# Optimization experiments

Hardware: AMD Instinct MI355X
Metric: run time of the kernel (lower is better)

The kernel has to match this reference:

```python
import jax, jax.numpy as jnp
import numpy as np

N_NODES = 50000


def gcn_conv(x, W, b, src, dst, n):
    """PyG-style GCNConv: symmetric-normalized aggregation over A + I.
    x: [N, Fin], W: [Fin, Fout], b: [Fout], src/dst: [E] int edge endpoints.
    """
    h = x @ W  # [N, Fout]
    # degree with self-loops: deg[i] = 1 + in-degree(i)
    deg = jnp.zeros((n,), dtype=h.dtype).at[dst].add(1.0) + 1.0
    dinv = jax.lax.rsqrt(deg)  # deg^-1/2
    norm_e = dinv[src] * dinv[dst]  # [E]
    # message passing: sum_j norm_ij * h_j  (plus self-loop term deg_i^-1 * h_i)
    agg = jnp.zeros_like(h).at[dst].add(h[src] * norm_e[:, None])
    agg = agg + h * (dinv * dinv)[:, None]
    return agg + b


def setup_inputs() -> dict:
    key = jax.random.key(0)
    ks = jax.random.split(key, 9)
    N, F_in, H, C = N_NODES, 128, 64, 4
    E = 1600000
    node_features = jax.random.normal(ks[0], (N, F_in), dtype=jnp.float32)
    edge_index = jax.random.randint(ks[1], (2, E), 0, N, dtype=jnp.int32)
    s1 = 1.0 / np.sqrt(F_in)
    s2 = 1.0 / np.sqrt(H)
    W1 = jax.random.uniform(ks[2], (F_in, H), jnp.float32, -s1, s1)
    b1 = jax.random.uniform(ks[3], (H,), jnp.float32, -s1, s1)
    W2 = jax.random.uniform(ks[4], (H, H), jnp.float32, -s2, s2)
    b2 = jax.random.uniform(ks[5], (H,), jnp.float32, -s2, s2)
    W3 = jax.random.uniform(ks[6], (H, C), jnp.float32, -s2, s2)
    b3 = jax.random.uniform(ks[7], (C,), jnp.float32, -s2, s2)
    return {"node_features": node_features, "edge_index": edge_index,
            "W1": W1, "b1": b1, "W2": W2, "b2": b2, "W3": W3, "b3": b3}


def reference(node_features, edge_index, W1, b1, W2, b2, W3, b3):
    n = node_features.shape[0]
    src, dst = edge_index[0], edge_index[1]
    out = jax.nn.relu(gcn_conv(node_features, W1, b1, src, dst, n))
    # layer2 applied 7 times with SHARED weights (faithful to the source)
    for _ in range(7):
        out = jax.nn.relu(gcn_conv(out, W2, b2, src, dst, n))
    out = gcn_conv(out, W3, b3, src, dst, n)
    return jax.nn.softmax(out, axis=0)  # softmax over the node dimension (dim=0)
```

## Files before the change

kernel.cpp:

```cpp
#include <hip/hip_runtime.h>
#include <hip/hip_fp16.h>
#include <math.h>
#include <float.h>


#define NPART 8
#define BPP   104

typedef float f4 __attribute__((ext_vector_type(4)));


__global__ __launch_bounds__(256) void k_count(const int* __restrict__ dst,
                                               unsigned* __restrict__ deg,
                                               int E, int chunk) {
    int part = blockIdx.x & (NPART - 1);
    int q = blockIdx.x >> 3;
    int lo = part * chunk, hi = lo + chunk;
    for (int e = q * 256 + threadIdx.x; e < E; e += 256 * BPP) {
        int d = dst[e];
        if (d >= lo && d < hi) atomicAdd(&deg[d], 1u);
    }
}

__global__ __launch_bounds__(256) void k_dinv(const unsigned* __restrict__ deg,
                                              float* __restrict__ dinv, int n) {
    int i = blockIdx.x * 256 + threadIdx.x;
    if (i < n) dinv[i] = rsqrtf(1.0f + (float)deg[i]);
}

__global__ __launch_bounds__(256) void k_scan1(const unsigned* __restrict__ deg,
                                               int* __restrict__ row_start,
                                               unsigned* __restrict__ bsum, int n) {
    __shared__ unsigned t[256];
    int i = blockIdx.x * 256 + threadIdx.x;
    unsigned v = (i < n) ? deg[i] : 0u;
    t[threadIdx.x] = v;
    __syncthreads();
    #pragma unroll
    for (int off = 1; off < 256; off <<= 1) {
        unsigned u = (threadIdx.x >= (unsigned)off) ? t[threadIdx.x - off] : 0u;
        __syncthreads();
        t[threadIdx.x] += u;
        __syncthreads();
    }
    if (i < n) row_start[i] = (int)(t[threadIdx.x] - v);
    if (threadIdx.x == 255) bsum[blockIdx.x] = t[255];
}

__global__ __launch_bounds__(256) void k_scan2(unsigned* __restrict__ bsum,
                                               int* __restrict__ row_start,
                                               int nb, int n) {
    __shared__ unsigned t[256];
    unsigned v = (threadIdx.x < (unsigned)nb) ? bsum[threadIdx.x] : 0u;
    t[threadIdx.x] = v;
    __syncthreads();
    #pragma unroll
    for (int off = 1; off < 256; off <<= 1) {
        unsigned u = (threadIdx.x >= (unsigned)off) ? t[threadIdx.x - off] : 0u;
        __syncthreads();
        t[threadIdx.x] += u;
        __syncthreads();
    }
    if (threadIdx.x < (unsigned)nb) bsum[threadIdx.x] = t[threadIdx.x] - v;
    if (threadIdx.x == 255) row_start[n] = (int)t[255];
}

__global__ __launch_bounds__(256) void k_scan3(int* __restrict__ row_start,
                                               const unsigned* __restrict__ bsum, int n) {
    int i = blockIdx.x * 256 + threadIdx.x;
    if (i < n) row_start[i] += (int)bsum[blockIdx.x];
}

__global__ __launch_bounds__(256) void k_fill(const int* __restrict__ src,
                                              const int* __restrict__ dst,
                                              const int* __restrict__ row_start,
                                              unsigned* __restrict__ cursor,
                                              int* __restrict__ csr_src,
                                              int E, int chunk) {
    int part = blockIdx.x & (NPART - 1);
    int q = blockIdx.x >> 3;
    int lo = part * chunk, hi = lo + chunk;
    for (int e = q * 256 + threadIdx.x; e < E; e += 256 * BPP) {
        int d = dst[e];
        if (d >= lo && d < hi) {
            int s = src[e];
            unsigned pos = atomicAdd(&cursor[d], 1u);
            csr_src[row_start[d] + (int)pos] = s;
        }
    }
}


__global__ __launch_bounds__(256) void k_gemm64_f32(const float* __restrict__ x,
                                                    const float* __restrict__ W,
                                                    const float* __restrict__ dinv,
                                                    __half* __restrict__ hs, int n) {
    __shared__ float Wl[128 * 64];
    {
        const f4* Wv = (const f4*)W;
        f4* Wlv = (f4*)Wl;
        for (int idx = threadIdx.x; idx < 128 * 16; idx += 256) Wlv[idx] = Wv[idx];
    }
    __syncthreads();
    int wave = threadIdx.x >> 6, lane = threadIdx.x & 63;
    int i0 = blockIdx.x * 16 + wave * 4;
    if (i0 >= n) return;
    if (i0 + 3 < n) {
        const f4* r0 = (const f4*)(x + (size_t)(i0 + 0) * 128);
        const f4* r1 = (const f4*)(x + (size_t)(i0 + 1) * 128);
        const f4* r2 = (const f4*)(x + (size_t)(i0 + 2) * 128);
        const f4* r3 = (const f4*)(x + (size_t)(i0 + 3) * 128);
        float a0 = 0.f, a1 = 0.f, a2 = 0.f, a3 = 0.f;
        #pragma unroll
        for (int k4 = 0; k4 < 32; ++k4) {
            f4 v0 = __builtin_nontemporal_load(&r0[k4]);
            f4 v1 = __builtin_nontemporal_load(&r1[k4]);
            f4 v2 = __builtin_nontemporal_load(&r2[k4]);
            f4 v3 = __builtin_nontemporal_load(&r3[k4]);
            float w0 = Wl[(k4 * 4 + 0) * 64 + lane];
            float w1 = Wl[(k4 * 4 + 1) * 64 + lane];
            float w2 = Wl[(k4 * 4 + 2) * 64 + lane];
            float w3 = Wl[(k4 * 4 + 3) * 64 + lane];
            a0 += v0.x * w0 + v0.y * w1 + v0.z * w2 + v0.w * w3;
            a1 += v1.x * w0 + v1.y * w1 + v1.z * w2 + v1.w * w3;
            a2 += v2.x * w0 + v2.y * w1 + v2.z * w2 + v2.w * w3;
            a3 += v3.x * w0 + v3.y * w1 + v3.z * w2 + v3.w * w3;
        }
        hs[(size_t)(i0 + 0) * 64 + lane] = __float2half(a0 * dinv[i0 + 0]);
        hs[(size_t)(i0 + 1) * 64 + lane] = __float2half(a1 * dinv[i0 + 1]);
        hs[(size_t)(i0 + 2) * 64 + lane] = __float2half(a2 * dinv[i0 + 2]);
        hs[(size_t)(i0 + 3) * 64 + lane] = __float2half(a3 * dinv[i0 + 3]);
    } else {
        for (int i = i0; i < n && i < i0 + 4; ++i) {
            const f4* r = (const f4*)(x + (size_t)i * 128);
            float acc = 0.f;
            #pragma unroll
            for (int k4 = 0; k4 < 32; ++k4) {
                f4 v = r[k4];
                acc += v.x * Wl[(k4 * 4 + 0) * 64 + lane];
                acc += v.y * Wl[(k4 * 4 + 1) * 64 + lane];
                acc += v.z * Wl[(k4 * 4 + 2) * 64 + lane];
                acc += v.w * Wl[(k4 * 4 + 3) * 64 + lane];
            }
            hs[(size_t)i * 64 + lane] = __float2half(acc * dinv[i]);
        }
    }
}


__global__ __launch_bounds__(256) void k_gemm64_f16(const __half* __restrict__ xh,
                                                    const float* __restrict__ W,
                                                    const float* __restrict__ dinv,
                                                    __half* __restrict__ hs, int n) {
    __shared__ float Wl[64 * 64];
    {
        const f4* Wv = (const f4*)W;
        f4* Wlv = (f4*)Wl;
        for (int idx = threadIdx.x; idx < 64 * 16; idx += 256) Wlv[idx] = Wv[idx];
    }
    __syncthreads();
    int wave = threadIdx.x >> 6, lane = threadIdx.x & 63;
    int i0 = blockIdx.x * 16 + wave * 4;
    if (i0 >= n) return;
    if (i0 + 3 < n) {
        const unsigned* r0 = (const unsigned*)(xh + (size_t)(i0 + 0) * 64);
        const unsigned* r1 = (const unsigned*)(xh + (size_t)(i0 + 1) * 64);
        const unsigned* r2 = (const unsigned*)(xh + (size_t)(i0 + 2) * 64);
        const unsigned* r3 = (const unsigned*)(xh + (size_t)(i0 + 3) * 64);
        float a0 = 0.f, a1 = 0.f, a2 = 0.f, a3 = 0.f;
        #pragma unroll
        for (int k2 = 0; k2 < 32; ++k2) {
            unsigned u0 = __builtin_nontemporal_load(&r0[k2]);
            unsigned u1 = __builtin_nontemporal_load(&r1[k2]);
            unsigned u2 = __builtin_nontemporal_load(&r2[k2]);
            unsigned u3 = __builtin_nontemporal_load(&r3[k2]);
            float w0 = Wl[(k2 * 2 + 0) * 64 + lane];
            float w1 = Wl[(k2 * 2 + 1) * 64 + lane];
            float2 v0 = __half22float2(*(__half2*)&u0);
            float2 v1 = __half22float2(*(__half2*)&u1);
            float2 v2 = __half22float2(*(__half2*)&u2);
            float2 v3 = __half22float2(*(__half2*)&u3);
            a0 += v0.x * w0 + v0.y * w1;
            a1 += v1.x * w0 + v1.y * w1;
            a2 += v2.x * w0 + v2.y * w1;
            a3 += v3.x * w0 + v3.y * w1;
        }
        hs[(size_t)(i0 + 0) * 64 + lane] = __float2half(a0 * dinv[i0 + 0]);
        hs[(size_t)(i0 + 1) * 64 + lane] = __float2half(a1 * dinv[i0 + 1]);
        hs[(size_t)(i0 + 2) * 64 + lane] = __float2half(a2 * dinv[i0 + 2]);
        hs[(size_t)(i0 + 3) * 64 + lane] = __float2half(a3 * dinv[i0 + 3]);
    } else {
        for (int i = i0; i < n && i < i0 + 4; ++i) {
            const __half2* r = (const __half2*)(xh + (size_t)i * 64);
            float acc = 0.f;
            #pragma unroll
            for (int k2 = 0; k2 < 32; ++k2) {
                float2 v = __half22float2(r[k2]);
                acc += v.x * Wl[(k2 * 2 + 0) * 64 + lane];
                acc += v.y * Wl[(k2 * 2 + 1) * 64 + lane];
            }
            hs[(size_t)i * 64 + lane] = __float2half(acc * dinv[i]);
        }
    }
}

__global__ __launch_bounds__(256) void k_gemm4(const __half* __restrict__ xh,
                                               const float* __restrict__ W,
                                               const float* __restrict__ dinv,
                                               float4* __restrict__ h4, int n) {
    __shared__ float Wl[256];
    for (int idx = threadIdx.x; idx < 256; idx += 256) Wl[idx] = W[idx];
    __syncthreads();
    int i = blockIdx.x * 256 + threadIdx.x;
    if (i >= n) return;
    const __half2* ar = (const __half2*)(xh + (size_t)i * 64);
    float a0 = 0.f, a1 = 0.f, a2 = 0.f, a3 = 0.f;
    #pragma unroll
    for (int k2 = 0; k2 < 32; ++k2) {
        float2 v = __half22float2(ar[k2]);
        int k = k2 * 2;
        a0 += v.x * Wl[k * 4 + 0] + v.y * Wl[(k + 1) * 4 + 0];
        a1 += v.x * Wl[k * 4 + 1] + v.y * Wl[(k + 1) * 4 + 1];
        a2 += v.x * Wl[k * 4 + 2] + v.y * Wl[(k + 1) * 4 + 2];
        a3 += v.x * Wl[k * 4 + 3] + v.y * Wl[(k + 1) * 4 + 3];
    }
    float di = dinv[i];
    h4[i] = make_float4(a0 * di, a1 * di, a2 * di, a3 * di);
}


__global__ __launch_bounds__(256) void k_agg64h(const __half* __restrict__ hs,
                                                const float* __restrict__ dinv,
                                                const int* __restrict__ row_start,
                                                const int* __restrict__ csr_src,
                                                const float* __restrict__ bias,
                                                __half* __restrict__ out, int n) {
    int wid = __builtin_amdgcn_readfirstlane((int)(threadIdx.x >> 6));
    int lane = threadIdx.x & 63;
    int gw = blockIdx.x * 4 + wid;
    if (gw >= n) return;
    float acc = __half2float(hs[(size_t)gw * 64 + lane]);
    int s = row_start[gw], e = row_start[gw + 1];
    int slot = s;
    for (; slot + 16 <= e; slot += 16) {
        int idx[16];
        #pragma unroll
        for (int j = 0; j < 16; ++j) idx[j] = csr_src[slot + j];
        float v[16];
        #pragma unroll
        for (int j = 0; j < 16; ++j) v[j] = __half2float(hs[(size_t)idx[j] * 64 + lane]);
        float t0 = ((v[0] + v[1]) + (v[2] + v[3])) + ((v[4] + v[5]) + (v[6] + v[7]));
        float t1 = ((v[8] + v[9]) + (v[10] + v[11])) + ((v[12] + v[13]) + (v[14] + v[15]));
        acc += t0 + t1;
    }
    for (; slot + 4 <= e; slot += 4) {
        int i0 = csr_src[slot + 0];
        int i1 = csr_src[slot + 1];
        int i2 = csr_src[slot + 2];
        int i3 = csr_src[slot + 3];
        float v0 = __half2float(hs[(size_t)i0 * 64 + lane]);
        float v1 = __half2float(hs[(size_t)i1 * 64 + lane]);
        float v2 = __half2float(hs[(size_t)i2 * 64 + lane]);
        float v3 = __half2float(hs[(size_t)i3 * 64 + lane]);
        acc += (v0 + v1) + (v2 + v3);
    }
    for (; slot < e; ++slot)
        acc += __half2float(hs[(size_t)csr_src[slot] * 64 + lane]);
    acc = acc * dinv[gw] + bias[lane];
    out[(size_t)gw * 64 + lane] = __float2half(fmaxf(acc, 0.f));
}


__global__ __launch_bounds__(256) void k_agg4(const float4* __restrict__ h4,
                                              const float* __restrict__ dinv,
                                              const int* __restrict__ row_start,
                                              const int* __restrict__ csr_src,
                                              const float* __restrict__ b3,
                                              float4* __restrict__ z, int n) {
    int i = blockIdx.x * 256 + threadIdx.x;
    if (i >= n) return;
    float4 self = h4[i];
    float a0 = self.x, a1 = self.y, a2 = self.z, a3 = self.w;
    int s = row_start[i], e = row_start[i + 1];
    int slot = s;
    for (; slot + 4 <= e; slot += 4) {
        int s0 = csr_src[slot + 0];
        int s1 = csr_src[slot + 1];
        int s2 = csr_src[slot + 2];
        int s3 = csr_src[slot + 3];
        float4 v0 = h4[s0], v1 = h4[s1], v2 = h4[s2], v3 = h4[s3];
        a0 += v0.x + v1.x + v2.x + v3.x;
        a1 += v0.y + v1.y + v2.y + v3.y;
        a2 += v0.z + v1.z + v2.z + v3.z;
        a3 += v0.w + v1.w + v2.w + v3.w;
    }
    for (; slot < e; ++slot) {
        float4 v = h4[csr_src[slot]];
        a0 += v.x; a1 += v.y; a2 += v.z; a3 += v.w;
    }
    float di = dinv[i];
    z[i] = make_float4(a0 * di + b3[0], a1 * di + b3[1],
                       a2 * di + b3[2], a3 * di + b3[3]);
}


__device__ inline unsigned encf(float f) {
    unsigned u = __float_as_uint(f);
    return (u & 0x80000000u) ? ~u : (u | 0x80000000u);
}
__device__ inline float decf(unsigned e) {
    return (e & 0x80000000u) ? __uint_as_float(e & 0x7FFFFFFFu) : __uint_as_float(~e);
}

__global__ __launch_bounds__(256) void k_max(const float4* __restrict__ z,
                                             unsigned* __restrict__ gmax, int n) {
    float m0 = -FLT_MAX, m1 = -FLT_MAX, m2 = -FLT_MAX, m3 = -FLT_MAX;
    for (int i = blockIdx.x * 256 + threadIdx.x; i < n; i += gridDim.x * 256) {
        float4 v = z[i];
        m0 = fmaxf(m0, v.x); m1 = fmaxf(m1, v.y);
        m2 = fmaxf(m2, v.z); m3 = fmaxf(m3, v.w);
    }
    #pragma unroll
    for (int off = 32; off; off >>= 1) {
        m0 = fmaxf(m0, __shfl_xor(m0, off));
        m1 = fmaxf(m1, __shfl_xor(m1, off));
        m2 = fmaxf(m2, __shfl_xor(m2, off));
        m3 = fmaxf(m3, __shfl_xor(m3, off));
    }
    if ((threadIdx.x & 63) == 0) {
        atomicMax(&gmax[0], encf(m0));
        atomicMax(&gmax[1], encf(m1));
        atomicMax(&gmax[2], encf(m2));
        atomicMax(&gmax[3], encf(m3));
    }
}

__global__ __launch_bounds__(256) void k_exp(const float4* __restrict__ z,
                                             float4* __restrict__ out,
                                             const unsigned* __restrict__ gmax,
                                             float* __restrict__ gsum, int n) {
    float M0 = decf(gmax[0]), M1 = decf(gmax[1]), M2 = decf(gmax[2]), M3 = decf(gmax[3]);
    float s0 = 0.f, s1 = 0.f, s2 = 0.f, s3 = 0.f;
    for (int i = blockIdx.x * 256 + threadIdx.x; i < n; i += gridDim.x * 256) {
        float4 v = z[i];
        float4 e;
        e.x = expf(v.x - M0); e.y = expf(v.y - M1);
        e.z = expf(v.z - M2); e.w = expf(v.w - M3);
        out[i] = e;
        s0 += e.x; s1 += e.y; s2 += e.z; s3 += e.w;
    }
    #pragma unroll
    for (int off = 32; off; off >>= 1) {
        s0 += __shfl_xor(s0, off);
        s1 += __shfl_xor(s1, off);
        s2 += __shfl_xor(s2, off);
        s3 += __shfl_xor(s3, off);
    }
    if ((threadIdx.x & 63) == 0) {
        atomicAdd(&gsum[0], s0);
        atomicAdd(&gsum[1], s1);
        atomicAdd(&gsum[2], s2);
        atomicAdd(&gsum[3], s3);
    }
}

__global__ __launch_bounds__(256) void k_norm(float4* __restrict__ out,
                                              const float* __restrict__ gsum, int n) {
    float r0 = 1.f / gsum[0], r1 = 1.f / gsum[1], r2 = 1.f / gsum[2], r3 = 1.f / gsum[3];
    for (int i = blockIdx.x * 256 + threadIdx.x; i < n; i += gridDim.x * 256) {
        float4 v = out[i];
        v.x *= r0; v.y *= r1; v.z *= r2; v.w *= r3;
        out[i] = v;
    }
}


extern "C" void kernel_launch(void* const* d_in, const int* in_sizes, int n_in,
                              void* d_out, int out_size, void* d_ws, size_t ws_size,
                              hipStream_t stream) {
    const float* x0 = (const float*)d_in[0];
    const int* ei = (const int*)d_in[1];
    const float* W1 = (const float*)d_in[2];
    const float* b1 = (const float*)d_in[3];
    const float* W2 = (const float*)d_in[4];
    const float* b2 = (const float*)d_in[5];
    const float* W3 = (const float*)d_in[6];
    const float* b3 = (const float*)d_in[7];

    const int n = in_sizes[0] / 128;
    const int E = in_sizes[1] / 2;
    const int* src = ei;
    const int* dst = ei + E;
    const int chunk = (n + NPART - 1) / NPART;

    char* ws = (char*)d_ws;
    size_t off = 0;
    auto alloc = [&](size_t bytes) -> void* {
        void* p = (void*)(ws + off);
        off = (off + bytes + 255) & ~(size_t)255;
        return p;
    };

    unsigned* deg    = (unsigned*)alloc((size_t)n * 4);
    unsigned* cursor = (unsigned*)alloc((size_t)n * 4);
    unsigned* gmax   = (unsigned*)alloc(16);
    float*    gsum   = (float*)alloc(16);
    size_t zero_bytes = off;

    float* dinv      = (float*)alloc((size_t)n * 4);
    int*   row_start = (int*)alloc((size_t)(n + 1) * 4);
    unsigned* bsum   = (unsigned*)alloc(1024 * 4);
    int*   csr_src   = (int*)alloc((size_t)E * 4);
    __half* hbuf     = (__half*)alloc((size_t)n * 64 * 2);
    __half* xbuf     = (__half*)alloc((size_t)n * 64 * 2);
    float4* h4buf    = (float4*)alloc((size_t)n * 16);
    float4* zbuf     = (float4*)alloc((size_t)n * 16);

    hipMemsetAsync(deg, 0, zero_bytes, stream);

    const int nbN = (n + 255) / 256;

    k_count<<<NPART * BPP, 256, 0, stream>>>(dst, deg, E, chunk);
    k_dinv<<<nbN, 256, 0, stream>>>(deg, dinv, n);
    k_scan1<<<nbN, 256, 0, stream>>>(deg, row_start, bsum, n);
    k_scan2<<<1, 256, 0, stream>>>(bsum, row_start, nbN, n);
    k_scan3<<<nbN, 256, 0, stream>>>(row_start, bsum, n);
    k_fill<<<NPART * BPP, 256, 0, stream>>>(src, dst, row_start, cursor, csr_src, E, chunk);

    const int nbG = (n + 15) / 16;
    const int nbA = (n + 3) / 4;

    k_gemm64_f32<<<nbG, 256, 0, stream>>>(x0, W1, dinv, hbuf, n);
    k_agg64h<<<nbA, 256, 0, stream>>>(hbuf, dinv, row_start, csr_src, b1, xbuf, n);

    for (int l = 0; l < 7; ++l) {
        k_gemm64_f16<<<nbG, 256, 0, stream>>>(xbuf, W2, dinv, hbuf, n);
        k_agg64h<<<nbA, 256, 0, stream>>>(hbuf, dinv, row_start, csr_src, b2, xbuf, n);
    }

    k_gemm4<<<nbN, 256, 0, stream>>>(xbuf, W3, dinv, h4buf, n);
    k_agg4<<<nbN, 256, 0, stream>>>(h4buf, dinv, row_start, csr_src, b3, zbuf, n);

    k_max<<<256, 256, 0, stream>>>(zbuf, gmax, n);
    k_exp<<<256, 256, 0, stream>>>(zbuf, (float4*)d_out, gmax, gsum, n);
    k_norm<<<256, 256, 0, stream>>>((float4*)d_out, gsum, n);
}
```

Baseline: 857.3 us.

## Split 64-wide half features into two 32-wide planes for aggregation passes

The GEMM kernels now write the scaled features as two planar halves (features 0-31 and 32-63), each n×32. Aggregation becomes two passes, one per plane, and each pass splits a wave into two 32-lane halves that gather alternate edges. A shuffle then combines the two partial sums. The goal is to shrink each gather pass's working set (about 3.2MB per plane) so it stays cache-resident. The cost is twice the kernel launches, twice the index reads, and 64-byte gathers instead of 128-byte ones.

After: 1.156 ms. +34.8%, slower.

```diff
diff --git a/kernel.cpp b/kernel.cpp
--- a/kernel.cpp
+++ b/kernel.cpp
@@ -103,6 +103,8 @@
     }
     __syncthreads();
     int wave = threadIdx.x >> 6, lane = threadIdx.x & 63;
+    size_t po = (lane >= 32) ? (size_t)n * 32 : 0;
+    int fl = lane & 31;
     int i0 = blockIdx.x * 16 + wave * 4;
     if (i0 >= n) return;
     if (i0 + 3 < n) {
@@ -126,10 +128,10 @@
             a2 += v2.x * w0 + v2.y * w1 + v2.z * w2 + v2.w * w3;
             a3 += v3.x * w0 + v3.y * w1 + v3.z * w2 + v3.w * w3;
         }
-        hs[(size_t)(i0 + 0) * 64 + lane] = __float2half(a0 * dinv[i0 + 0]);
-        hs[(size_t)(i0 + 1) * 64 + lane] = __float2half(a1 * dinv[i0 + 1]);
-        hs[(size_t)(i0 + 2) * 64 + lane] = __float2half(a2 * dinv[i0 + 2]);
-        hs[(size_t)(i0 + 3) * 64 + lane] = __float2half(a3 * dinv[i0 + 3]);
+        hs[po + (size_t)(i0 + 0) * 32 + fl] = __float2half(a0 * dinv[i0 + 0]);
+        hs[po + (size_t)(i0 + 1) * 32 + fl] = __float2half(a1 * dinv[i0 + 1]);
+        hs[po + (size_t)(i0 + 2) * 32 + fl] = __float2half(a2 * dinv[i0 + 2]);
+        hs[po + (size_t)(i0 + 3) * 32 + fl] = __float2half(a3 * dinv[i0 + 3]);
     } else {
         for (int i = i0; i < n && i < i0 + 4; ++i) {
             const f4* r = (const f4*)(x + (size_t)i * 128);
@@ -142,7 +144,7 @@
                 acc += v.z * Wl[(k4 * 4 + 2) * 64 + lane];
                 acc += v.w * Wl[(k4 * 4 + 3) * 64 + lane];
             }
-            hs[(size_t)i * 64 + lane] = __float2half(acc * dinv[i]);
+            hs[po + (size_t)i * 32 + fl] = __float2half(acc * dinv[i]);
         }
     }
 }
@@ -160,6 +162,8 @@
     }
     __syncthreads();
     int wave = threadIdx.x >> 6, lane = threadIdx.x & 63;
+    size_t po = (lane >= 32) ? (size_t)n * 32 : 0;
+    int fl = lane & 31;
     int i0 = blockIdx.x * 16 + wave * 4;
     if (i0 >= n) return;
     if (i0 + 3 < n) {
@@ -185,10 +189,10 @@
             a2 += v2.x * w0 + v2.y * w1;
             a3 += v3.x * w0 + v3.y * w1;
         }
-        hs[(size_t)(i0 + 0) * 64 + lane] = __float2half(a0 * dinv[i0 + 0]);
-        hs[(size_t)(i0 + 1) * 64 + lane] = __float2half(a1 * dinv[i0 + 1]);
-        hs[(size_t)(i0 + 2) * 64 + lane] = __float2half(a2 * dinv[i0 + 2]);
-        hs[(size_t)(i0 + 3) * 64 + lane] = __float2half(a3 * dinv[i0 + 3]);
+        hs[po + (size_t)(i0 + 0) * 32 + fl] = __float2half(a0 * dinv[i0 + 0]);
+        hs[po + (size_t)(i0 + 1) * 32 + fl] = __float2half(a1 * dinv[i0 + 1]);
+        hs[po + (size_t)(i0 + 2) * 32 + fl] = __float2half(a2 * dinv[i0 + 2]);
+        hs[po + (size_t)(i0 + 3) * 32 + fl] = __float2half(a3 * dinv[i0 + 3]);
     } else {
         for (int i = i0; i < n && i < i0 + 4; ++i) {
             const __half2* r = (const __half2*)(xh + (size_t)i * 64);
@@ -199,7 +203,7 @@
                 acc += v.x * Wl[(k2 * 2 + 0) * 64 + lane];
                 acc += v.y * Wl[(k2 * 2 + 1) * 64 + lane];
             }
-            hs[(size_t)i * 64 + lane] = __float2half(acc * dinv[i]);
+            hs[po + (size_t)i * 32 + fl] = __float2half(acc * dinv[i]);
         }
     }
 }
@@ -229,45 +233,37 @@
 }
 
 
-__global__ __launch_bounds__(256) void k_agg64h(const __half* __restrict__ hs,
-                                                const float* __restrict__ dinv,
-                                                const int* __restrict__ row_start,
-                                                const int* __restrict__ csr_src,
-                                                const float* __restrict__ bias,
-                                                __half* __restrict__ out, int n) {
-    int wid = __builtin_amdgcn_readfirstlane((int)(threadIdx.x >> 6));
+__global__ __launch_bounds__(256) void k_agg32(const __half* __restrict__ plane,
+                                               const float* __restrict__ dinv,
+                                               const int* __restrict__ row_start,
+                                               const int* __restrict__ csr_src,
+                                               const float* __restrict__ biasP,
+                                               __half* __restrict__ outP, int n) {
+    int wid = threadIdx.x >> 6;
     int lane = threadIdx.x & 63;
+    int sub = lane >> 5;
+    int fl = lane & 31;
     int gw = blockIdx.x * 4 + wid;
     if (gw >= n) return;
-    float acc = __half2float(hs[(size_t)gw * 64 + lane]);
+    float acc = (sub == 0) ? __half2float(plane[(size_t)gw * 32 + fl]) : 0.f;
     int s = row_start[gw], e = row_start[gw + 1];
-    int slot = s;
-    for (; slot + 16 <= e; slot += 16) {
-        int idx[16];
+    int sb = s;
+    for (; sb + 16 <= e; sb += 16) {
+        float v[8];
         #pragma unroll
-        for (int j = 0; j < 16; ++j) idx[j] = csr_src[slot + j];
-        float v[16];
-        #pragma unroll
-        for (int j = 0; j < 16; ++j) v[j] = __half2float(hs[(size_t)idx[j] * 64 + lane]);
-        float t0 = ((v[0] + v[1]) + (v[2] + v[3])) + ((v[4] + v[5]) + (v[6] + v[7]));
-        float t1 = ((v[8] + v[9]) + (v[10] + v[11])) + ((v[12] + v[13]) + (v[14] + v[15]));
-        acc += t0 + t1;
-    }
-    for (; slot + 4 <= e; slot += 4) {
-        int i0 = csr_src[slot + 0];
-        int i1 = csr_src[slot + 1];
-        int i2 = csr_src[slot + 2];
-        int i3 = csr_src[slot + 3];
-        float v0 = __half2float(hs[(size_t)i0 * 64 + lane]);
-        float v1 = __half2float(hs[(size_t)i1 * 64 + lane]);
-        float v2 = __half2float(hs[(size_t)i2 * 64 + lane]);
-        float v3 = __half2float(hs[(size_t)i3 * 64 + lane]);
-        acc += (v0 + v1) + (v2 + v3);
-    }
-    for (; slot < e; ++slot)
-        acc += __half2float(hs[(size_t)csr_src[slot] * 64 + lane]);
-    acc = acc * dinv[gw] + bias[lane];
-    out[(size_t)gw * 64 + lane] = __float2half(fmaxf(acc, 0.f));
+        for (int k = 0; k < 8; ++k) {
+            int idx = csr_src[sb + 2 * k + sub];
+            v[k] = __half2float(plane[(size_t)idx * 32 + fl]);
+        }
+        acc += ((v[0] + v[1]) + (v[2] + v[3])) + ((v[4] + v[5]) + (v[6] + v[7]));
+    }
+    for (int t = sb + sub; t < e; t += 2)
+        acc += __half2float(plane[(size_t)csr_src[t] * 32 + fl]);
+    acc += __shfl_xor(acc, 32);
+    if (sub == 0) {
+        acc = acc * dinv[gw] + biasP[fl];
+        outP[(size_t)gw * 64 + fl] = __float2half(fmaxf(acc, 0.f));
+    }
 }
 
 
@@ -430,12 +426,17 @@
     const int nbG = (n + 15) / 16;
     const int nbA = (n + 3) / 4;
 
+    __half* plane0 = hbuf;
+    __half* plane1 = hbuf + (size_t)n * 32;
+
     k_gemm64_f32<<<nbG, 256, 0, stream>>>(x0, W1, dinv, hbuf, n);
-    k_agg64h<<<nbA, 256, 0, stream>>>(hbuf, dinv, row_start, csr_src, b1, xbuf, n);
+    k_agg32<<<nbA, 256, 0, stream>>>(plane0, dinv, row_start, csr_src, b1,      xbuf,      n);
+    k_agg32<<<nbA, 256, 0, stream>>>(plane1, dinv, row_start, csr_src, b1 + 32, xbuf + 32, n);
 
     for (int l = 0; l < 7; ++l) {
         k_gemm64_f16<<<nbG, 256, 0, stream>>>(xbuf, W2, dinv, hbuf, n);
-        k_agg64h<<<nbA, 256, 0, stream>>>(hbuf, dinv, row_start, csr_src, b2, xbuf, n);
+        k_agg32<<<nbA, 256, 0, stream>>>(plane0, dinv, row_start, csr_src, b2,      xbuf,      n);
+        k_agg32<<<nbA, 256, 0, stream>>>(plane1, dinv, row_start, csr_src, b2 + 32, xbuf + 32, n);
     }
 
     k_gemm4<<<nbN, 256, 0, stream>>>(xbuf, W3, dinv, h4buf, n);
```

## Bucket CSR neighbor lists by source-node range within each row

Applied to the files above, without the earlier changes.

Builds the CSR with each destination row split into four sub-buckets keyed by which quarter of the node range the source lies in, so neighbor indices in each row are roughly grouped by source region. The intent is better cache locality for the gathered feature rows during the nine aggregation passes. The cost is a four-times-larger count/cursor/offset array, a longer multi-pass scan, and a count kernel that now runs over all edges with one atomic each. The aggregation kernels still read only the row's first and last offsets, so their logic is unchanged.

Result: no change. 845.3 us (-1.4%).

```diff
diff --git a/kernel.cpp b/kernel.cpp
--- a/kernel.cpp
+++ b/kernel.cpp
@@ -6,34 +6,35 @@
 
 #define NPART 8
 #define BPP   104
+#define T     4
 
 typedef float f4 __attribute__((ext_vector_type(4)));
 
 
-__global__ __launch_bounds__(256) void k_count(const int* __restrict__ dst,
-                                               unsigned* __restrict__ deg,
-                                               int E, int chunk) {
-    int part = blockIdx.x & (NPART - 1);
-    int q = blockIdx.x >> 3;
-    int lo = part * chunk, hi = lo + chunk;
-    for (int e = q * 256 + threadIdx.x; e < E; e += 256 * BPP) {
-        int d = dst[e];
-        if (d >= lo && d < hi) atomicAdd(&deg[d], 1u);
-    }
-}
-
-__global__ __launch_bounds__(256) void k_dinv(const unsigned* __restrict__ deg,
+__global__ __launch_bounds__(256) void k_count(const int* __restrict__ src,
+                                               const int* __restrict__ dst,
+                                               unsigned* __restrict__ cnt,
+                                               int E, int chunkS) {
+    int e = blockIdx.x * 256 + threadIdx.x;
+    if (e >= E) return;
+    int d = dst[e];
+    int t = src[e] / chunkS;
+    atomicAdd(&cnt[d * T + t], 1u);
+}
+
+__global__ __launch_bounds__(256) void k_dinv(const int* __restrict__ rowt,
                                               float* __restrict__ dinv, int n) {
     int i = blockIdx.x * 256 + threadIdx.x;
-    if (i < n) dinv[i] = rsqrtf(1.0f + (float)deg[i]);
-}
-
-__global__ __launch_bounds__(256) void k_scan1(const unsigned* __restrict__ deg,
-                                               int* __restrict__ row_start,
-                                               unsigned* __restrict__ bsum, int n) {
+    if (i < n) dinv[i] = rsqrtf(1.0f + (float)(rowt[i * T + T] - rowt[i * T]));
+}
+
+
+__global__ __launch_bounds__(256) void k_scan1(const unsigned* __restrict__ cnt,
+                                               int* __restrict__ rowt,
+                                               unsigned* __restrict__ bsum, int m) {
     __shared__ unsigned t[256];
     int i = blockIdx.x * 256 + threadIdx.x;
-    unsigned v = (i < n) ? deg[i] : 0u;
+    unsigned v = (i < m) ? cnt[i] : 0u;
     t[threadIdx.x] = v;
     __syncthreads();
     #pragma unroll
@@ -43,40 +44,48 @@
         t[threadIdx.x] += u;
         __syncthreads();
     }
-    if (i < n) row_start[i] = (int)(t[threadIdx.x] - v);
+    if (i < m) rowt[i] = (int)(t[threadIdx.x] - v);
     if (threadIdx.x == 255) bsum[blockIdx.x] = t[255];
 }
 
 __global__ __launch_bounds__(256) void k_scan2(unsigned* __restrict__ bsum,
-                                               int* __restrict__ row_start,
-                                               int nb, int n) {
+                                               int* __restrict__ rowt,
+                                               int nb, int m, int E) {
     __shared__ unsigned t[256];
-    unsigned v = (threadIdx.x < (unsigned)nb) ? bsum[threadIdx.x] : 0u;
-    t[threadIdx.x] = v;
-    __syncthreads();
-    #pragma unroll
-    for (int off = 1; off < 256; off <<= 1) {
-        unsigned u = (threadIdx.x >= (unsigned)off) ? t[threadIdx.x - off] : 0u;
+    unsigned run = 0;
+    for (int base = 0; base < nb; base += 256) {
+        int i = base + threadIdx.x;
+        unsigned v = (i < nb) ? bsum[i] : 0u;
+        t[threadIdx.x] = v;
         __syncthreads();
-        t[threadIdx.x] += u;
+        #pragma unroll
+        for (int off = 1; off < 256; off <<= 1) {
+            unsigned u = (threadIdx.x >= (unsigned)off) ? t[threadIdx.x - off] : 0u;
+            __syncthreads();
+            t[threadIdx.x] += u;
+            __syncthreads();
+        }
+        if (i < nb) bsum[i] = run + t[threadIdx.x] - v;
         __syncthreads();
-    }
-    if (threadIdx.x < (unsigned)nb) bsum[threadIdx.x] = t[threadIdx.x] - v;
-    if (threadIdx.x == 255) row_start[n] = (int)t[255];
-}
-
-__global__ __launch_bounds__(256) void k_scan3(int* __restrict__ row_start,
-                                               const unsigned* __restrict__ bsum, int n) {
+        run += t[255];
+        __syncthreads();
+    }
+    if (threadIdx.x == 0) rowt[m] = E;
+}
+
+__global__ __launch_bounds__(256) void k_scan3(int* __restrict__ rowt,
+                                               const unsigned* __restrict__ bsum, int m) {
     int i = blockIdx.x * 256 + threadIdx.x;
-    if (i < n) row_start[i] += (int)bsum[blockIdx.x];
-}
+    if (i < m) rowt[i] += (int)bsum[blockIdx.x];
+}
+
 
 __global__ __launch_bounds__(256) void k_fill(const int* __restrict__ src,
                                               const int* __restrict__ dst,
-                                              const int* __restrict__ row_start,
+                                              const int* __restrict__ rowt,
                                               unsigned* __restrict__ cursor,
                                               int* __restrict__ csr_src,
-                                              int E, int chunk) {
+                                              int E, int chunk, int chunkS) {
     int part = blockIdx.x & (NPART - 1);
     int q = blockIdx.x >> 3;
     int lo = part * chunk, hi = lo + chunk;
@@ -84,8 +93,9 @@
         int d = dst[e];
         if (d >= lo && d < hi) {
             int s = src[e];
-            unsigned pos = atomicAdd(&cursor[d], 1u);
-            csr_src[row_start[d] + (int)pos] = s;
+            int slot4 = d * T + s / chunkS;
+            unsigned pos = atomicAdd(&cursor[slot4], 1u);
+            csr_src[rowt[slot4] + (int)pos] = s;
         }
     }
 }
@@ -231,7 +241,7 @@
 
 __global__ __launch_bounds__(256) void k_agg64h(const __half* __restrict__ hs,
                                                 const float* __restrict__ dinv,
-                                                const int* __restrict__ row_start,
+                                                const int* __restrict__ rowt,
                                                 const int* __restrict__ csr_src,
                                                 const float* __restrict__ bias,
                                                 __half* __restrict__ out, int n) {
@@ -240,7 +250,7 @@
     int gw = blockIdx.x * 4 + wid;
     if (gw >= n) return;
     float acc = __half2float(hs[(size_t)gw * 64 + lane]);
-    int s = row_start[gw], e = row_start[gw + 1];
+    int s = rowt[gw * T], e = rowt[gw * T + T];
     int slot = s;
     for (; slot + 16 <= e; slot += 16) {
         int idx[16];
@@ -273,7 +283,7 @@
 
 __global__ __launch_bounds__(256) void k_agg4(const float4* __restrict__ h4,
                                               const float* __restrict__ dinv,
-                                              const int* __restrict__ row_start,
+                                              const int* __restrict__ rowt,
                                               const int* __restrict__ csr_src,
                                               const float* __restrict__ b3,
                                               float4* __restrict__ z, int n) {
@@ -281,7 +291,7 @@
     if (i >= n) return;
     float4 self = h4[i];
     float a0 = self.x, a1 = self.y, a2 = self.z, a3 = self.w;
-    int s = row_start[i], e = row_start[i + 1];
+    int s = rowt[i * T], e = rowt[i * T + T];
     int slot = s;
     for (; slot + 4 <= e; slot += 4) {
         int s0 = csr_src[slot + 0];
@@ -392,6 +402,8 @@
     const int* src = ei;
     const int* dst = ei + E;
     const int chunk = (n + NPART - 1) / NPART;
+    const int chunkS = (n + T - 1) / T;
+    const int m = n * T;
 
     char* ws = (char*)d_ws;
     size_t off = 0;
@@ -401,14 +413,14 @@
         return p;
     };
 
-    unsigned* deg    = (unsigned*)alloc((size_t)n * 4);
-    unsigned* cursor = (unsigned*)alloc((size_t)n * 4);
+    unsigned* cnt    = (unsigned*)alloc((size_t)m * 4);
+    unsigned* cursor = (unsigned*)alloc((size_t)m * 4);
     unsigned* gmax   = (unsigned*)alloc(16);
     float*    gsum   = (float*)alloc(16);
     size_t zero_bytes = off;
 
     float* dinv      = (float*)alloc((size_t)n * 4);
-    int*   row_start = (int*)alloc((size_t)(n + 1) * 4);
+    int*   rowt      = (int*)alloc((size_t)(m + 1) * 4);
     unsigned* bsum   = (unsigned*)alloc(1024 * 4);
     int*   csr_src   = (int*)alloc((size_t)E * 4);
     __half* hbuf     = (__half*)alloc((size_t)n * 64 * 2);
@@ -416,30 +428,32 @@
     float4* h4buf    = (float4*)alloc((size_t)n * 16);
     float4* zbuf     = (float4*)alloc((size_t)n * 16);
 
-    hipMemsetAsync(deg, 0, zero_bytes, stream);
+    hipMemsetAsync(cnt, 0, zero_bytes, stream);
 
     const int nbN = (n + 255) / 256;
-
-    k_count<<<NPART * BPP, 256, 0, stream>>>(dst, deg, E, chunk);
-    k_dinv<<<nbN, 256, 0, stream>>>(deg, dinv, n);
-    k_scan1<<<nbN, 256, 0, stream>>>(deg, row_start, bsum, n);
-    k_scan2<<<1, 256, 0, stream>>>(bsum, row_start, nbN, n);
-    k_scan3<<<nbN, 256, 0, stream>>>(row_start, bsum, n);
-    k_fill<<<NPART * BPP, 256, 0, stream>>>(src, dst, row_start, cursor, csr_src, E, chunk);
+    const int nbE = (E + 255) / 256;
+    const int nbM = (m + 255) / 256;
+
+    k_count<<<nbE, 256, 0, stream>>>(src, dst, cnt, E, chunkS);
+    k_scan1<<<nbM, 256, 0, stream>>>(cnt, rowt, bsum, m);
+    k_scan2<<<1, 256, 0, stream>>>(bsum, rowt, nbM, m, E);
+    k_scan3<<<nbM, 256, 0, stream>>>(rowt, bsum, m);
+    k_dinv<<<nbN, 256, 0, stream>>>(rowt, dinv, n);
+    k_fill<<<NPART * BPP, 256, 0, stream>>>(src, dst, rowt, cursor, csr_src, E, chunk, chunkS);
 
     const int nbG = (n + 15) / 16;
     const int nbA = (n + 3) / 4;
 
     k_gemm64_f32<<<nbG, 256, 0, stream>>>(x0, W1, dinv, hbuf, n);
-    k_agg64h<<<nbA, 256, 0, stream>>>(hbuf, dinv, row_start, csr_src, b1, xbuf, n);
+    k_agg64h<<<nbA, 256, 0, stream>>>(hbuf, dinv, rowt, csr_src, b1, xbuf, n);
 
     for (int l = 0; l < 7; ++l) {
         k_gemm64_f16<<<nbG, 256, 0, stream>>>(xbuf, W2, dinv, hbuf, n);
-        k_agg64h<<<nbA, 256, 0, stream>>>(hbuf, dinv, row_start, csr_src, b2, xbuf, n);
+        k_agg64h<<<nbA, 256, 0, stream>>>(hbuf, dinv, rowt, csr_src, b2, xbuf, n);
     }
 
     k_gemm4<<<nbN, 256, 0, stream>>>(xbuf, W3, dinv, h4buf, n);
-    k_agg4<<<nbN, 256, 0, stream>>>(h4buf, dinv, row_start, csr_src, b3, zbuf, n);
+    k_agg4<<<nbN, 256, 0, stream>>>(h4buf, dinv, rowt, csr_src, b3, zbuf, n);
 
     k_max<<<256, 256, 0, stream>>>(zbuf, gmax, n);
     k_exp<<<256, 256, 0, stream>>>(zbuf, (float4*)d_out, gmax, gsum, n);
```
